# Optimization experiments

Hardware: AMD Instinct MI355X
Metric: run time of the kernel (lower is better)

The kernel has to match this reference:

```python
import jax, jax.numpy as jnp
import numpy as np

B, Q, K, D, H = 8, 128, 1024, 256, 256


def setup_inputs() -> dict:
    key = jax.random.key(0)
    ks = jax.random.split(key, 7)
    queries = jax.random.normal(ks[0], (B, Q, D), dtype=jnp.float32)
    keys = jax.random.normal(ks[1], (B, K, D), dtype=jnp.float32)
    values = jax.random.normal(ks[2], (B, K, D), dtype=jnp.float32)
    W_q = jax.random.normal(ks[3], (H, D), dtype=jnp.float32) * (1.0 / np.sqrt(D))
    W_k = jax.random.normal(ks[4], (H, D), dtype=jnp.float32) * (1.0 / np.sqrt(D))
    w_v = jax.random.normal(ks[5], (H,), dtype=jnp.float32) * (1.0 / np.sqrt(H))
    valid_lens = jax.random.randint(ks[6], (B,), 0, K, dtype=jnp.int64)
    return {"queries": queries, "keys": keys, "values": values,
            "W_q": W_q, "W_k": W_k, "w_v": w_v, "valid_lens": valid_lens}


def reference(queries, keys, values, W_q, W_k, w_v, valid_lens):
    # Linear projections (bias=False): [B,Q,H], [B,K,H]
    q = jnp.einsum("bqd,hd->bqh", queries, W_q)
    k = jnp.einsum("bkd,hd->bkh", keys, W_k)
    # Broadcast add -> tanh -> reduce with w_v: scores [B,Q,K]
    features = jnp.tanh(q[:, :, None, :] + k[:, None, :, :])  # [B,Q,K,H]
    scores = jnp.einsum("bqkh,h->bqk", features, w_v)
    # Masked softmax over K: positions >= valid_len get -1e9
    mask = jnp.arange(K)[None, None, :] < valid_lens[:, None, None]
    scores = jnp.where(mask, scores, jnp.float32(-1e9))
    attn = jax.nn.softmax(scores, axis=-1)  # [B,Q,K]
    # Dropout p=0.0 (eval): identity. bmm(attn, values) -> [B,Q,Dv]
    return jnp.einsum("bqk,bkv->bqv", attn, values)
```

## Files before the change

### kernel.cpp

```cpp
#include <hip/hip_runtime.h>

#define BB 8
#define QQ 128
#define KK 1024
#define DD 256
#define HH 256

#define KSP 32
#define KCH 32

#define ZSP 4
#define RTOT (BB * QQ + BB * KK)
#define PSTRIDE ((size_t)RTOT * HH)

#define TWO_LOG2E     2.8853900817779268f
#define NEG_TWO_LOG2E -2.8853900817779268f

__global__ __launch_bounds__(256) void proj_kernel(const float* __restrict__ queries,
                                                   const float* __restrict__ keys,
                                                   const float* __restrict__ Wq,
                                                   const float* __restrict__ Wk,
                                                   const int* __restrict__ vlen,
                                                   float* __restrict__ pp) {
    const int r0 = blockIdx.x * 64;
    const bool isQ = (r0 < BB * QQ);
    if (!isQ) {
        const int kb = (r0 - BB * QQ) >> 6;
        const int b  = kb >> 4;
        const int k0 = (kb & 15) << 6;
        if (k0 >= vlen[b]) return;
    }

    __shared__ float smem[2 * 64 * 68];
    float (*As)[68] = (float(*)[68])smem;
    float (*Ws)[68] = (float(*)[68])(smem + 64 * 68);

    const int t  = threadIdx.x;
    const int tr = t & 15;
    const int th = t >> 4;
    const int h0 = blockIdx.y * 64;
    const int dc = blockIdx.z * 64;
    const float* A = isQ ? (queries + (size_t)r0 * DD)
                         : (keys + (size_t)(r0 - BB * QQ) * DD);
    const float* W = isQ ? Wq : Wk;

#pragma unroll
    for (int i = 0; i < 4; ++i) {
        int fi  = t + 256 * i;
        int row = fi >> 4;
        int c4  = (fi & 15) << 2;
        *(float4*)&As[row][c4] = *(const float4*)&A[(size_t)row * DD + dc + c4];
        *(float4*)&Ws[row][c4] = *(const float4*)&W[(size_t)(h0 + row) * DD + dc + c4];
    }
    __syncthreads();

    float acc[4][4] = {};
#pragma unroll 2
    for (int dd = 0; dd < 64; dd += 4) {
        float4 a4[4], w4[4];
#pragma unroll
        for (int i = 0; i < 4; ++i) a4[i] = *(float4*)&As[tr + 16 * i][dd];
#pragma unroll
        for (int j = 0; j < 4; ++j) w4[j] = *(float4*)&Ws[th + 16 * j][dd];
#pragma unroll
        for (int i = 0; i < 4; ++i)
#pragma unroll
            for (int j = 0; j < 4; ++j) {
                acc[i][j] += a4[i].x * w4[j].x + a4[i].y * w4[j].y +
                             a4[i].z * w4[j].z + a4[i].w * w4[j].w;
            }
    }
    __syncthreads();

    float (*Ob)[68] = (float(*)[68])smem;
#pragma unroll
    for (int i = 0; i < 4; ++i)
#pragma unroll
        for (int j = 0; j < 4; ++j)
            Ob[tr + 16 * i][th + 16 * j] = TWO_LOG2E * acc[i][j];
    __syncthreads();

    float* outp = pp + (size_t)blockIdx.z * PSTRIDE + (size_t)r0 * HH + h0;
#pragma unroll
    for (int i = 0; i < 4; ++i) {
        int fi  = t + 256 * i;
        int row = fi >> 4;
        int c4  = (fi & 15) << 2;
        *(float4*)&outp[(size_t)row * HH + c4] = *(float4*)&Ob[row][c4];
    }
}

__global__ __launch_bounds__(256) void combine_kernel(const float* __restrict__ pp,
                                                      const int* __restrict__ vlen,
                                                      float* __restrict__ ppc) {
    const int row = blockIdx.x * 4 + (threadIdx.x >> 6);
    const int l   = threadIdx.x & 63;
    if (row >= BB * QQ) {
        const int rk = row - BB * QQ;
        const int b  = rk >> 10;
        const int k  = rk & (KK - 1);
        if (k >= vlen[b]) return;
    }
    const float* base = pp + (size_t)row * HH + (l << 2);
    float4 v0 = *(const float4*)base;
    float4 v1 = *(const float4*)(base + PSTRIDE);
    float4 v2 = *(const float4*)(base + 2 * PSTRIDE);
    float4 v3 = *(const float4*)(base + 3 * PSTRIDE);
    float4 s;
    s.x = __builtin_amdgcn_exp2f((v0.x + v1.x) + (v2.x + v3.x));
    s.y = __builtin_amdgcn_exp2f((v0.y + v1.y) + (v2.y + v3.y));
    s.z = __builtin_amdgcn_exp2f((v0.z + v1.z) + (v2.z + v3.z));
    s.w = __builtin_amdgcn_exp2f((v0.w + v1.w) + (v2.w + v3.w));
    *(float4*)&ppc[(size_t)row * HH + (l << 2)] = s;
}

__global__ __launch_bounds__(512, 4) void scoreav_kernel(const float* __restrict__ ppc,
                                                         const float* __restrict__ wv,
                                                         const int* __restrict__ vlen,
                                                         const float* __restrict__ V,
                                                         float* __restrict__ partial,
                                                         float* __restrict__ psum) {
    int id = blockIdx.x;
    int b = 0;
    bool found = false;
#pragma unroll
    for (int bb = 0; bb < BB; ++bb) {
        if (!found) {
            int v = vlen[bb];
            int cnt = ((v == 0) ? KSP : ((v + KCH - 1) / KCH)) * 4;
            if (id < cnt) { b = bb; found = true; }
            else id -= cnt;
        }
    }
    if (!found) return;
    const int ksb = id >> 2;
    const int q0  = (id & 3) * 32;
    const int k0  = ksb * KCH;
    const int vl  = vlen[b];

    __shared__ float st[2][32][260];
    __shared__ float pT[KCH][36];
    float* red = &st[0][0][0];

    const int t = threadIdx.x;
    const int w = t >> 6;
    const int l = t & 63;
    const int ql = l & 7;
    const int kl = l >> 3;

    float acc[4][4] = {};

    if (vl > 0) {
#pragma unroll
        for (int i = 0; i < 8; ++i) {
            int fi  = t + 512 * i;
            int row = fi >> 6;
            int c4  = (fi & 63) << 2;
            size_t gr = (row < 32) ? (size_t)(b * QQ + q0 + row)
                                   : (size_t)(BB * QQ + b * KK + k0 + row - 32);
            *(float4*)&st[row >> 5][row & 31][c4] =
                *(const float4*)&ppc[gr * HH + c4];
        }
        __syncthreads();

        const int hw = 32 * w;
#pragma unroll
        for (int hh = 0; hh < 32; hh += 4) {
            const float4 w4 = *(const float4*)&wv[hw + hh];
            const float* wa = (const float*)&w4;
            float4 q4[4], k4[4];
#pragma unroll
            for (int i = 0; i < 4; ++i) q4[i] = *(float4*)&st[0][ql + 8 * i][hw + hh];
#pragma unroll
            for (int j = 0; j < 4; ++j) k4[j] = *(float4*)&st[1][kl + 8 * j][hw + hh];
#pragma unroll
            for (int i = 0; i < 4; ++i) {
                const float* qa = (const float*)&q4[i];
#pragma unroll
                for (int j = 0; j < 4; ++j) {
                    const float* ka = (const float*)&k4[j];
#pragma unroll
                    for (int c = 0; c < 4; ++c) {
                        float d = __builtin_fmaf(qa[c], ka[c], 1.0f);
                        acc[i][j] += wa[c] * __builtin_amdgcn_rcpf(d);
                    }
                }
            }
        }
        __syncthreads();

#pragma unroll
        for (int i = 0; i < 4; ++i)
#pragma unroll
            for (int j = 0; j < 4; ++j)
                red[w * 1056 + (ql + 8 * i) * 33 + (kl + 8 * j)] = acc[i][j];
    }
    __syncthreads();

    float pvv[2];
#pragma unroll
    for (int u = 0; u < 2; ++u) {
        int n = t + 512 * u;
        int q = n >> 5, k = n & 31;
        float s = 0.f;
        if (vl > 0) {
#pragma unroll
            for (int ww = 0; ww < 8; ++ww) s += red[ww * 1056 + q * 33 + k];
        }
        int kg = k0 + k;
        float pv;
        if (vl == 0) pv = 1.0f;
        else pv = (kg < vl) ? __builtin_amdgcn_exp2f(NEG_TWO_LOG2E * s) : 0.0f;
        pT[k][q] = pv;
        pvv[u] = pv;
    }
    float s0 = pvv[0], s1 = pvv[1];
#pragma unroll
    for (int off = 1; off < 32; off <<= 1) {
        s0 += __shfl_xor(s0, off);
        s1 += __shfl_xor(s1, off);
    }
    if ((l & 31) == 0) {
        int qa = 2 * w + (l >> 5);
        psum[((size_t)ksb * BB + b) * QQ + q0 + qa]      = s0;
        psum[((size_t)ksb * BB + b) * QQ + q0 + qa + 16] = s1;
    }
    __syncthreads();

    const float* VB = V + ((size_t)b * KK + k0) * DD;
    const int d4 = (t & 63) << 2;
    const int qg = w << 2;
    float4 a4[4] = {};
#pragma unroll 4
    for (int k = 0; k < KCH; ++k) {
        float4 v4 = *(const float4*)&VB[(size_t)k * DD + d4];
        float4 p4 = *(float4*)&pT[k][qg];
        a4[0].x += p4.x * v4.x; a4[0].y += p4.x * v4.y; a4[0].z += p4.x * v4.z; a4[0].w += p4.x * v4.w;
        a4[1].x += p4.y * v4.x; a4[1].y += p4.y * v4.y; a4[1].z += p4.y * v4.z; a4[1].w += p4.y * v4.w;
        a4[2].x += p4.z * v4.x; a4[2].y += p4.z * v4.y; a4[2].z += p4.z * v4.z; a4[2].w += p4.z * v4.w;
        a4[3].x += p4.w * v4.x; a4[3].y += p4.w * v4.y; a4[3].z += p4.w * v4.z; a4[3].w += p4.w * v4.w;
    }
#pragma unroll
    for (int qi = 0; qi < 4; ++qi) {
        int q = q0 + qg + qi;
        *(float4*)&partial[(((size_t)ksb * BB + b) * QQ + q) * DD + d4] = a4[qi];
    }
}

__global__ __launch_bounds__(256) void av_reduce(const float* __restrict__ partial,
                                                 const float* __restrict__ psum,
                                                 const int* __restrict__ vlen,
                                                 float* __restrict__ out) {
    const int i  = blockIdx.x * 256 + threadIdx.x;
    const int bq = i >> 6;
    const int b  = bq >> 7;
    const int vl = vlen[b];
    const int nch = (vl == 0) ? KSP : ((vl + KCH - 1) / KCH);

    const float4* p4 = (const float4*)partial;
    const int stride4 = BB * QQ * DD / 4;

    float S = 0.f;
    float4 s = {0.f, 0.f, 0.f, 0.f};
    int ks = 0;
    for (; ks + 4 <= nch; ks += 4) {
        float Sa = psum[(size_t)(ks + 0) * (BB * QQ) + bq];
        float Sb = psum[(size_t)(ks + 1) * (BB * QQ) + bq];
        float Sc = psum[(size_t)(ks + 2) * (BB * QQ) + bq];
        float Sd = psum[(size_t)(ks + 3) * (BB * QQ) + bq];
        float4 x0 = p4[(size_t)(ks + 0) * stride4 + i];
        float4 x1 = p4[(size_t)(ks + 1) * stride4 + i];
        float4 x2 = p4[(size_t)(ks + 2) * stride4 + i];
        float4 x3 = p4[(size_t)(ks + 3) * stride4 + i];
        S += (Sa + Sb) + (Sc + Sd);
        s.x += (x0.x + x1.x) + (x2.x + x3.x);
        s.y += (x0.y + x1.y) + (x2.y + x3.y);
        s.z += (x0.z + x1.z) + (x2.z + x3.z);
        s.w += (x0.w + x1.w) + (x2.w + x3.w);
    }
    for (; ks < nch; ++ks) {
        S += psum[(size_t)ks * (BB * QQ) + bq];
        float4 x = p4[(size_t)ks * stride4 + i];
        s.x += x.x; s.y += x.y; s.z += x.z; s.w += x.w;
    }

    const float inv = 1.0f / S;
    s.x *= inv; s.y *= inv; s.z *= inv; s.w *= inv;
    ((float4*)out)[i] = s;
}

extern "C" void kernel_launch(void* const* d_in, const int* in_sizes, int n_in,
                              void* d_out, int out_size, void* d_ws, size_t ws_size,
                              hipStream_t stream) {
    const float* queries = (const float*)d_in[0];
    const float* keys    = (const float*)d_in[1];
    const float* values  = (const float*)d_in[2];
    const float* W_q     = (const float*)d_in[3];
    const float* W_k     = (const float*)d_in[4];
    const float* w_v     = (const float*)d_in[5];
    const int*   vlen    = (const int*)d_in[6];
    float* out = (float*)d_out;

    float* ws      = (float*)d_ws;
    float* pp      = ws;
    float* ppc     = pp + (size_t)ZSP * PSTRIDE;
    float* psum    = ppc + PSTRIDE;
    float* partial = psum + (size_t)KSP * BB * QQ;

    proj_kernel<<<dim3(RTOT / 64, HH / 64, ZSP), 256, 0, stream>>>(
        queries, keys, W_q, W_k, vlen, pp);

    combine_kernel<<<dim3(RTOT / 4, 1, 1), 256, 0, stream>>>(pp, vlen, ppc);

    scoreav_kernel<<<dim3(KSP * 4 * BB, 1, 1), 512, 0, stream>>>(
        ppc, w_v, vlen, values, partial, psum);

    av_reduce<<<dim3(BB * QQ * DD / 4 / 256, 1, 1), 256, 0, stream>>>(
        partial, psum, vlen, out);
}
```

Before: 127.6 us.

## Halve scoreav block to 256 threads, stage H in two halves

```diff
diff --git a/kernel.cpp b/kernel.cpp
--- a/kernel.cpp
+++ b/kernel.cpp
@@ -114,12 +114,12 @@
     *(float4*)&ppc[(size_t)row * HH + (l << 2)] = s;
 }
 
-__global__ __launch_bounds__(512, 4) void scoreav_kernel(const float* __restrict__ ppc,
-                                                         const float* __restrict__ wv,
-                                                         const int* __restrict__ vlen,
-                                                         const float* __restrict__ V,
-                                                         float* __restrict__ partial,
-                                                         float* __restrict__ psum) {
+__global__ __launch_bounds__(256) void scoreav_kernel(const float* __restrict__ ppc,
+                                                      const float* __restrict__ wv,
+                                                      const int* __restrict__ vlen,
+                                                      const float* __restrict__ V,
+                                                      float* __restrict__ partial,
+                                                      float* __restrict__ psum) {
     int id = blockIdx.x;
     int b = 0;
     bool found = false;
@@ -138,7 +138,7 @@
     const int k0  = ksb * KCH;
     const int vl  = vlen[b];
 
-    __shared__ float st[2][32][260];
+    __shared__ float st[2][32][132];
     __shared__ float pT[KCH][36];
     float* red = &st[0][0][0];
 
@@ -152,42 +152,46 @@
 
     if (vl > 0) {
 #pragma unroll
-        for (int i = 0; i < 8; ++i) {
-            int fi  = t + 512 * i;
-            int row = fi >> 6;
-            int c4  = (fi & 63) << 2;
-            size_t gr = (row < 32) ? (size_t)(b * QQ + q0 + row)
-                                   : (size_t)(BB * QQ + b * KK + k0 + row - 32);
-            *(float4*)&st[row >> 5][row & 31][c4] =
-                *(const float4*)&ppc[gr * HH + c4];
-        }
-        __syncthreads();
-
-        const int hw = 32 * w;
-#pragma unroll
-        for (int hh = 0; hh < 32; hh += 4) {
-            const float4 w4 = *(const float4*)&wv[hw + hh];
-            const float* wa = (const float*)&w4;
-            float4 q4[4], k4[4];
-#pragma unroll
-            for (int i = 0; i < 4; ++i) q4[i] = *(float4*)&st[0][ql + 8 * i][hw + hh];
-#pragma unroll
-            for (int j = 0; j < 4; ++j) k4[j] = *(float4*)&st[1][kl + 8 * j][hw + hh];
-#pragma unroll
-            for (int i = 0; i < 4; ++i) {
-                const float* qa = (const float*)&q4[i];
-#pragma unroll
-                for (int j = 0; j < 4; ++j) {
-                    const float* ka = (const float*)&k4[j];
-#pragma unroll
-                    for (int c = 0; c < 4; ++c) {
-                        float d = __builtin_fmaf(qa[c], ka[c], 1.0f);
-                        acc[i][j] += wa[c] * __builtin_amdgcn_rcpf(d);
+        for (int half = 0; half < 2; ++half) {
+            const int hbase = 128 * half;
+#pragma unroll
+            for (int i = 0; i < 8; ++i) {
+                int fi  = t + 256 * i;
+                int row = fi >> 5;
+                int c4  = (fi & 31) << 2;
+                size_t gr = (row < 32) ? (size_t)(b * QQ + q0 + row)
+                                       : (size_t)(BB * QQ + b * KK + k0 + row - 32);
+                *(float4*)&st[row >> 5][row & 31][c4] =
+                    *(const float4*)&ppc[gr * HH + hbase + c4];
+            }
+            __syncthreads();
+
+            const int hl = 32 * w;
+#pragma unroll
+            for (int hh = 0; hh < 32; hh += 4) {
+                const float4 w4 = *(const float4*)&wv[hbase + hl + hh];
+                const float* wa = (const float*)&w4;
+                float4 q4[4], k4[4];
+#pragma unroll
+                for (int i = 0; i < 4; ++i) q4[i] = *(float4*)&st[0][ql + 8 * i][hl + hh];
+#pragma unroll
+                for (int j = 0; j < 4; ++j) k4[j] = *(float4*)&st[1][kl + 8 * j][hl + hh];
+#pragma unroll
+                for (int i = 0; i < 4; ++i) {
+                    const float* qa = (const float*)&q4[i];
+#pragma unroll
+                    for (int j = 0; j < 4; ++j) {
+                        const float* ka = (const float*)&k4[j];
+#pragma unroll
+                        for (int c = 0; c < 4; ++c) {
+                            float d = __builtin_fmaf(qa[c], ka[c], 1.0f);
+                            acc[i][j] += wa[c] * __builtin_amdgcn_rcpf(d);
+                        }
                     }
                 }
             }
-        }
-        __syncthreads();
+            __syncthreads();
+        }
 
 #pragma unroll
         for (int i = 0; i < 4; ++i)
@@ -197,15 +201,15 @@
     }
     __syncthreads();
 
-    float pvv[2];
-#pragma unroll
-    for (int u = 0; u < 2; ++u) {
-        int n = t + 512 * u;
+    float pvv[4];
+#pragma unroll
+    for (int u = 0; u < 4; ++u) {
+        int n = t + 256 * u;
         int q = n >> 5, k = n & 31;
         float s = 0.f;
         if (vl > 0) {
 #pragma unroll
-            for (int ww = 0; ww < 8; ++ww) s += red[ww * 1056 + q * 33 + k];
+            for (int ww = 0; ww < 4; ++ww) s += red[ww * 1056 + q * 33 + k];
         }
         int kg = k0 + k;
         float pv;
@@ -214,34 +218,45 @@
         pT[k][q] = pv;
         pvv[u] = pv;
     }
-    float s0 = pvv[0], s1 = pvv[1];
 #pragma unroll
     for (int off = 1; off < 32; off <<= 1) {
-        s0 += __shfl_xor(s0, off);
-        s1 += __shfl_xor(s1, off);
+#pragma unroll
+        for (int u = 0; u < 4; ++u) pvv[u] += __shfl_xor(pvv[u], off);
     }
     if ((l & 31) == 0) {
-        int qa = 2 * w + (l >> 5);
-        psum[((size_t)ksb * BB + b) * QQ + q0 + qa]      = s0;
-        psum[((size_t)ksb * BB + b) * QQ + q0 + qa + 16] = s1;
+#pragma unroll
+        for (int u = 0; u < 4; ++u) {
+            int qa = 2 * w + 8 * u + (l >> 5);
+            psum[((size_t)ksb * BB + b) * QQ + q0 + qa] = pvv[u];
+        }
     }
     __syncthreads();
 
     const float* VB = V + ((size_t)b * KK + k0) * DD;
     const int d4 = (t & 63) << 2;
-    const int qg = w << 2;
-    float4 a4[4] = {};
+    const int qg = w << 3;
+    float4 a4[8] = {{0.f,0.f,0.f,0.f},{0.f,0.f,0.f,0.f},{0.f,0.f,0.f,0.f},{0.f,0.f,0.f,0.f},
+                    {0.f,0.f,0.f,0.f},{0.f,0.f,0.f,0.f},{0.f,0.f,0.f,0.f},{0.f,0.f,0.f,0.f}};
 #pragma unroll 4
     for (int k = 0; k < KCH; ++k) {
         float4 v4 = *(const float4*)&VB[(size_t)k * DD + d4];
-        float4 p4 = *(float4*)&pT[k][qg];
-        a4[0].x += p4.x * v4.x; a4[0].y += p4.x * v4.y; a4[0].z += p4.x * v4.z; a4[0].w += p4.x * v4.w;
-        a4[1].x += p4.y * v4.x; a4[1].y += p4.y * v4.y; a4[1].z += p4.y * v4.z; a4[1].w += p4.y * v4.w;
-        a4[2].x += p4.z * v4.x; a4[2].y += p4.z * v4.y; a4[2].z += p4.z * v4.z; a4[2].w += p4.z * v4.w;
-        a4[3].x += p4.w * v4.x; a4[3].y += p4.w * v4.y; a4[3].z += p4.w * v4.z; a4[3].w += p4.w * v4.w;
-    }
-#pragma unroll
-    for (int qi = 0; qi < 4; ++qi) {
+        float4 pA = *(float4*)&pT[k][qg];
+        float4 pB = *(float4*)&pT[k][qg + 4];
+        const float* pa = (const float*)&pA;
+        const float* pb = (const float*)&pB;
+#pragma unroll
+        for (int qi = 0; qi < 4; ++qi) {
+            a4[qi].x += pa[qi] * v4.x; a4[qi].y += pa[qi] * v4.y;
+            a4[qi].z += pa[qi] * v4.z; a4[qi].w += pa[qi] * v4.w;
+        }
+#pragma unroll
+        for (int qi = 0; qi < 4; ++qi) {
+            a4[4 + qi].x += pb[qi] * v4.x; a4[4 + qi].y += pb[qi] * v4.y;
+            a4[4 + qi].z += pb[qi] * v4.z; a4[4 + qi].w += pb[qi] * v4.w;
+        }
+    }
+#pragma unroll
+    for (int qi = 0; qi < 8; ++qi) {
         int q = q0 + qg + qi;
         *(float4*)&partial[(((size_t)ksb * BB + b) * QQ + q) * DD + d4] = a4[qi];
     }
@@ -312,7 +327,7 @@
 
     combine_kernel<<<dim3(RTOT / 4, 1, 1), 256, 0, stream>>>(pp, vlen, ppc);
 
-    scoreav_kernel<<<dim3(KSP * 4 * BB, 1, 1), 512, 0, stream>>>(
+    scoreav_kernel<<<dim3(KSP * 4 * BB, 1, 1), 256, 0, stream>>>(
         ppc, w_v, vlen, values, partial, psum);
 
     av_reduce<<<dim3(BB * QQ * DD / 4 / 256, 1, 1), 256, 0, stream>>>(
```

After: 129.3 us. About the same (+1.3%).
